# Kernel tuning notes

Measured on AMD Instinct MI355X. Metric: run time of the kernel, lower is better.

Reference implementation:

```python
import jax, jax.numpy as jnp
import numpy as np

N_SRC = 200000
N_TGT = 40000
NNZ = 280000
D_IN = 256
D_OUT = 256
LN_EPS = 1e-5


def setup_inputs() -> dict:
    key = jax.random.key(0)
    ks = jax.random.split(key, 6)
    x = jax.random.normal(ks[0], (N_SRC, D_IN), dtype=jnp.float32)
    rows = jax.random.randint(ks[1], (NNZ,), 0, N_TGT, dtype=jnp.int32)
    cols = jax.random.randint(ks[2], (NNZ,), 0, N_SRC, dtype=jnp.int32)
    vals = jax.random.uniform(ks[3], (NNZ,), dtype=jnp.float32)
    # Linear(in_dim, out_dim) params (PyTorch-style init scale)
    W = jax.random.normal(ks[4], (D_IN, D_OUT), dtype=jnp.float32) / np.sqrt(D_IN)
    b = jnp.zeros((D_OUT,), dtype=jnp.float32)
    # LayerNorm(out_dim) params
    gamma = jnp.ones((D_OUT,), dtype=jnp.float32)
    beta = jnp.zeros((D_OUT,), dtype=jnp.float32)
    return {"x": x, "rows": rows, "cols": cols, "vals": vals,
            "W": W, "b": b, "gamma": gamma, "beta": beta,
            "num_targets": N_TGT}


def reference(x, rows, cols, vals, W, b, gamma, beta, num_targets):
    # SpMM: mapped[t, :] = sum_{e: rows[e]==t} vals[e] * x[cols[e], :]
    contrib = x[cols] * vals[:, None]                      # [nnz, d_in]
    mapped = jax.ops.segment_sum(contrib, rows, num_segments=num_targets)  # [n_tgt, d_in]
    # Linear
    h = mapped @ W + b                                     # [n_tgt, d_out]
    # LayerNorm
    mu = jnp.mean(h, axis=-1, keepdims=True)
    var = jnp.mean(jnp.square(h - mu), axis=-1, keepdims=True)
    normed = (h - mu) * jax.lax.rsqrt(var + LN_EPS) * gamma + beta
    # GELU (exact erf form, matches torch nn.GELU default)
    return jax.nn.gelu(normed, approximate=False)
```

## Files before the change

kernel.cpp:

```cpp
#include <hip/hip_runtime.h>
#include <math.h>

#define D 256
#define TM 32
#define KC 16
#define LN_EPS 1e-5f
#define SCAN_CHUNK 1024

__global__ __launch_bounds__(256) void hist_kernel(
    const int* __restrict__ rows, int* __restrict__ cnt, int nnz)
{
    const int e = blockIdx.x * 256 + threadIdx.x;
    if (e < nnz) atomicAdd(&cnt[rows[e]], 1);
}

__global__ __launch_bounds__(256) void scan1_kernel(
    const int* __restrict__ cnt, int* __restrict__ row_ptr,
    int* __restrict__ partials, int n)
{
    const int tid = threadIdx.x;
    const int base = blockIdx.x * SCAN_CHUNK + tid * 4;
    int v[4];
#pragma unroll
    for (int q = 0; q < 4; q++) {
        const int i = base + q;
        v[q] = (i < n) ? cnt[i] : 0;
    }
    const int tsum = v[0] + v[1] + v[2] + v[3];

    const int lane = tid & 63;
    int s = tsum;
#pragma unroll
    for (int off = 1; off < 64; off <<= 1) {
        const int t = __shfl_up(s, off);
        if (lane >= off) s += t;
    }
    __shared__ int wtot[4];
    if (lane == 63) wtot[tid >> 6] = s;
    __syncthreads();
    const int w = tid >> 6;
    int woff = 0;
#pragma unroll
    for (int u = 0; u < 4; u++) if (u < w) woff += wtot[u];

    int run = woff + s - tsum;
#pragma unroll
    for (int q = 0; q < 4; q++) {
        const int i = base + q;
        if (i < n) row_ptr[i] = run;
        run += v[q];
    }
    if (tid == 255) partials[blockIdx.x] = woff + s;
}

__global__ __launch_bounds__(64) void scan2_kernel(int* __restrict__ partials, int nb)
{
    const int t = threadIdx.x;
    const int v = (t < nb) ? partials[t] : 0;
    int s = v;
#pragma unroll
    for (int off = 1; off < 64; off <<= 1) {
        const int u = __shfl_up(s, off);
        if (t >= off) s += u;
    }
    if (t < nb) partials[t] = s - v;
}

__global__ __launch_bounds__(256) void scan3_kernel(
    int* __restrict__ row_ptr, int* __restrict__ cursor,
    const int* __restrict__ partials, int n, int nnz)
{
    const int tid = threadIdx.x;
    const int base = blockIdx.x * SCAN_CHUNK + tid * 4;
    const int add = partials[blockIdx.x];
#pragma unroll
    for (int q = 0; q < 4; q++) {
        const int i = base + q;
        if (i < n) {
            const int rp = row_ptr[i] + add;
            row_ptr[i] = rp;
            cursor[i]  = rp;
        }
    }
    if (blockIdx.x == 0 && tid == 0) row_ptr[n] = nnz;
}

__global__ __launch_bounds__(256) void reorder_kernel(
    const int* __restrict__ rows, const int* __restrict__ cols,
    const float* __restrict__ vals, int* __restrict__ cursor,
    int* __restrict__ scol, float* __restrict__ sval, int nnz)
{
    const int e = blockIdx.x * 256 + threadIdx.x;
    if (e < nnz) {
        const int r = rows[e];
        const int pos = atomicAdd(&cursor[r], 1);
        scol[pos] = cols[e];
        sval[pos] = vals[e];
    }
}

__global__ __launch_bounds__(256, 8) void gather_kernel(
    const float* __restrict__ x, const int* __restrict__ row_ptr,
    const int* __restrict__ scol, const float* __restrict__ sval,
    float* __restrict__ mapped, int n_tgt)
{
    const int wid = (int)((blockIdx.x * blockDim.x + threadIdx.x) >> 6);
    const int lane = threadIdx.x & 63;
    if (wid >= n_tgt) return;

    const int beg = row_ptr[wid];
    const int end = row_ptr[wid + 1];

    float4 a0 = make_float4(0.f, 0.f, 0.f, 0.f);
    float4 a1 = a0, a2 = a0, a3 = a0;

    int e = beg;
    for (; e + 4 <= end; e += 4) {
        const int c0 = scol[e], c1 = scol[e + 1], c2 = scol[e + 2], c3 = scol[e + 3];
        const float v0 = sval[e], v1 = sval[e + 1], v2 = sval[e + 2], v3 = sval[e + 3];
        const float4 x0 = *(const float4*)(x + (size_t)c0 * D + 4 * lane);
        const float4 x1 = *(const float4*)(x + (size_t)c1 * D + 4 * lane);
        const float4 x2 = *(const float4*)(x + (size_t)c2 * D + 4 * lane);
        const float4 x3 = *(const float4*)(x + (size_t)c3 * D + 4 * lane);
        a0.x = fmaf(v0, x0.x, a0.x); a0.y = fmaf(v0, x0.y, a0.y);
        a0.z = fmaf(v0, x0.z, a0.z); a0.w = fmaf(v0, x0.w, a0.w);
        a1.x = fmaf(v1, x1.x, a1.x); a1.y = fmaf(v1, x1.y, a1.y);
        a1.z = fmaf(v1, x1.z, a1.z); a1.w = fmaf(v1, x1.w, a1.w);
        a2.x = fmaf(v2, x2.x, a2.x); a2.y = fmaf(v2, x2.y, a2.y);
        a2.z = fmaf(v2, x2.z, a2.z); a2.w = fmaf(v2, x2.w, a2.w);
        a3.x = fmaf(v3, x3.x, a3.x); a3.y = fmaf(v3, x3.y, a3.y);
        a3.z = fmaf(v3, x3.z, a3.z); a3.w = fmaf(v3, x3.w, a3.w);
    }
    for (; e < end; e++) {
        const int c0 = scol[e];
        const float v0 = sval[e];
        const float4 x0 = *(const float4*)(x + (size_t)c0 * D + 4 * lane);
        a0.x = fmaf(v0, x0.x, a0.x); a0.y = fmaf(v0, x0.y, a0.y);
        a0.z = fmaf(v0, x0.z, a0.z); a0.w = fmaf(v0, x0.w, a0.w);
    }
    const float4 acc = make_float4(a0.x + a1.x + a2.x + a3.x,
                                   a0.y + a1.y + a2.y + a3.y,
                                   a0.z + a1.z + a2.z + a3.z,
                                   a0.w + a1.w + a2.w + a3.w);
    *(float4*)(mapped + (size_t)wid * D + 4 * lane) = acc;
}

__global__ __launch_bounds__(256) void gemm_ln_gelu_kernel(
    const float* __restrict__ mapped, const float* __restrict__ Wm,
    const float* __restrict__ bias, const float* __restrict__ gamma,
    const float* __restrict__ beta, float* __restrict__ out, int n_tgt)
{
    __shared__ float As[TM][KC + 4];
    __shared__ float Bs[KC][D];

    const int tid = threadIdx.x;
    const int tr = tid >> 5;
    const int tc = tid & 31;
    const int r0 = blockIdx.x * TM;

    float acc[4][8];
#pragma unroll
    for (int i = 0; i < 4; i++)
#pragma unroll
        for (int j = 0; j < 8; j++) acc[i][j] = 0.f;

    for (int k0 = 0; k0 < D; k0 += KC) {
        if (tid < 128) {
            const int a_row = tid >> 2;
            const int a_kq  = (tid & 3) * 4;
            const float4 av = *(const float4*)(mapped + (size_t)(r0 + a_row) * D + k0 + a_kq);
            *(float4*)&As[a_row][a_kq] = av;
        }
#pragma unroll
        for (int q = 0; q < 4; q++) {
            const int idx = q * 256 + tid;
            const int kk = idx >> 6;
            const int c4 = (idx & 63) * 4;
            *(float4*)&Bs[kk][c4] = *(const float4*)(Wm + (size_t)(k0 + kk) * D + c4);
        }
        __syncthreads();

#pragma unroll
        for (int q = 0; q < 4; q++) {
            float4 a4[4];
#pragma unroll
            for (int i = 0; i < 4; i++)
                a4[i] = *(const float4*)&As[tr * 4 + i][q * 4];
#pragma unroll
            for (int kk = 0; kk < 4; kk++) {
                const float4 b0 = *(const float4*)&Bs[q * 4 + kk][4 * tc];
                const float4 b1 = *(const float4*)&Bs[q * 4 + kk][128 + 4 * tc];
#pragma unroll
                for (int i = 0; i < 4; i++) {
                    const float ai = (kk == 0) ? a4[i].x :
                                     (kk == 1) ? a4[i].y :
                                     (kk == 2) ? a4[i].z : a4[i].w;
                    acc[i][0] = fmaf(ai, b0.x, acc[i][0]);
                    acc[i][1] = fmaf(ai, b0.y, acc[i][1]);
                    acc[i][2] = fmaf(ai, b0.z, acc[i][2]);
                    acc[i][3] = fmaf(ai, b0.w, acc[i][3]);
                    acc[i][4] = fmaf(ai, b1.x, acc[i][4]);
                    acc[i][5] = fmaf(ai, b1.y, acc[i][5]);
                    acc[i][6] = fmaf(ai, b1.z, acc[i][6]);
                    acc[i][7] = fmaf(ai, b1.w, acc[i][7]);
                }
            }
        }
        __syncthreads();
    }

    float gm[8], bt[8], bs[8];
#pragma unroll
    for (int j = 0; j < 8; j++) {
        const int c = (j < 4) ? (4 * tc + j) : (128 + 4 * tc + (j - 4));
        gm[j] = gamma[c]; bt[j] = beta[c]; bs[j] = bias[c];
    }

#pragma unroll
    for (int i = 0; i < 4; i++) {
        float s = 0.f, ss = 0.f;
#pragma unroll
        for (int j = 0; j < 8; j++) {
            const float h = acc[i][j] + bs[j];
            acc[i][j] = h;
            s += h; ss += h * h;
        }
#pragma unroll
        for (int off = 16; off > 0; off >>= 1) {
            s  += __shfl_xor(s,  off);
            ss += __shfl_xor(ss, off);
        }
        const float mean = s * (1.f / D);
        const float var  = ss * (1.f / D) - mean * mean;
        const float rstd = rsqrtf(var + LN_EPS);

        const int row = r0 + tr * 4 + i;
        float y[8];
#pragma unroll
        for (int j = 0; j < 8; j++) {
            const float v = (acc[i][j] - mean) * rstd * gm[j] + bt[j];
            y[j] = 0.5f * v * (1.f + erff(v * 0.70710678118654752f));
        }
        float* op = out + (size_t)row * D;
        *(float4*)(op + 4 * tc)       = make_float4(y[0], y[1], y[2], y[3]);
        *(float4*)(op + 128 + 4 * tc) = make_float4(y[4], y[5], y[6], y[7]);
    }
}

extern "C" void kernel_launch(void* const* d_in, const int* in_sizes, int n_in,
                              void* d_out, int out_size, void* d_ws, size_t ws_size,
                              hipStream_t stream) {
    const float* x     = (const float*)d_in[0];
    const int*   rows  = (const int*)d_in[1];
    const int*   cols  = (const int*)d_in[2];
    const float* vals  = (const float*)d_in[3];
    const float* Wm    = (const float*)d_in[4];
    const float* bias  = (const float*)d_in[5];
    const float* gamma = (const float*)d_in[6];
    const float* beta  = (const float*)d_in[7];
    float* out = (float*)d_out;

    const int nnz   = in_sizes[1];
    const int n_tgt = out_size / D;

    int* cnt      = (int*)d_ws;
    int* row_ptr  = cnt + n_tgt;
    int* cursor   = row_ptr + n_tgt + 1;
    int* partials = cursor + n_tgt;
    int* scol     = partials + 64;
    float* sval   = (float*)(scol + nnz);
    float* mapped = (float*)(sval + nnz);
    mapped = (float*)(((uintptr_t)mapped + 15) & ~(uintptr_t)15);

    hipMemsetAsync(cnt, 0, (size_t)n_tgt * sizeof(int), stream);

    const int eblocks = (nnz + 255) / 256;
    hist_kernel<<<eblocks, 256, 0, stream>>>(rows, cnt, nnz);

    const int sblocks = (n_tgt + SCAN_CHUNK - 1) / SCAN_CHUNK;
    scan1_kernel<<<sblocks, 256, 0, stream>>>(cnt, row_ptr, partials, n_tgt);
    scan2_kernel<<<1, 64, 0, stream>>>(partials, sblocks);
    scan3_kernel<<<sblocks, 256, 0, stream>>>(row_ptr, cursor, partials, n_tgt, nnz);

    reorder_kernel<<<eblocks, 256, 0, stream>>>(rows, cols, vals, cursor,
                                                scol, sval, nnz);

    const int wblocks = (n_tgt * 64 + 255) / 256;
    gather_kernel<<<wblocks, 256, 0, stream>>>(x, row_ptr, scol, sval,
                                               mapped, n_tgt);

    const int gblocks = n_tgt / TM;
    gemm_ln_gelu_kernel<<<gblocks, 256, 0, stream>>>(mapped, Wm, bias, gamma,
                                                     beta, out, n_tgt);
}
```

Baseline: 423.3 us.

## Fuse SpMM gather into GEMM+LayerNorm+GELU kernel via shared-memory tile

The gather kernel and the GEMM/LN/GELU kernel become one. Each block of 4 wavefronts gathers its 32 target rows straight into a full 32x256 shared-memory A tile, so the mapped intermediate is never written to or read back from global memory. Column indices and values are now loaded cooperatively 64 at a time and broadcast with lane shuffles instead of every lane reading them redundantly. The cost is a larger shared-memory footprint (As grows to 32KB), which lowers occupancy. The gather phase also loses the latency hiding that independent gather waves had, because each wave handles 8 rows serially before the GEMM can start.

Result: slower. 445.7 us (+5.3%).

```diff
diff --git a/kernel.cpp b/kernel.cpp
--- a/kernel.cpp
+++ b/kernel.cpp
@@ -99,64 +99,81 @@
     }
 }
 
-__global__ __launch_bounds__(256, 8) void gather_kernel(
+__global__ __launch_bounds__(256) void fused_spmm_gemm_kernel(
     const float* __restrict__ x, const int* __restrict__ row_ptr,
     const int* __restrict__ scol, const float* __restrict__ sval,
-    float* __restrict__ mapped, int n_tgt)
-{
-    const int wid = (int)((blockIdx.x * blockDim.x + threadIdx.x) >> 6);
-    const int lane = threadIdx.x & 63;
-    if (wid >= n_tgt) return;
-
-    const int beg = row_ptr[wid];
-    const int end = row_ptr[wid + 1];
-
-    float4 a0 = make_float4(0.f, 0.f, 0.f, 0.f);
-    float4 a1 = a0, a2 = a0, a3 = a0;
-
-    int e = beg;
-    for (; e + 4 <= end; e += 4) {
-        const int c0 = scol[e], c1 = scol[e + 1], c2 = scol[e + 2], c3 = scol[e + 3];
-        const float v0 = sval[e], v1 = sval[e + 1], v2 = sval[e + 2], v3 = sval[e + 3];
-        const float4 x0 = *(const float4*)(x + (size_t)c0 * D + 4 * lane);
-        const float4 x1 = *(const float4*)(x + (size_t)c1 * D + 4 * lane);
-        const float4 x2 = *(const float4*)(x + (size_t)c2 * D + 4 * lane);
-        const float4 x3 = *(const float4*)(x + (size_t)c3 * D + 4 * lane);
-        a0.x = fmaf(v0, x0.x, a0.x); a0.y = fmaf(v0, x0.y, a0.y);
-        a0.z = fmaf(v0, x0.z, a0.z); a0.w = fmaf(v0, x0.w, a0.w);
-        a1.x = fmaf(v1, x1.x, a1.x); a1.y = fmaf(v1, x1.y, a1.y);
-        a1.z = fmaf(v1, x1.z, a1.z); a1.w = fmaf(v1, x1.w, a1.w);
-        a2.x = fmaf(v2, x2.x, a2.x); a2.y = fmaf(v2, x2.y, a2.y);
-        a2.z = fmaf(v2, x2.z, a2.z); a2.w = fmaf(v2, x2.w, a2.w);
-        a3.x = fmaf(v3, x3.x, a3.x); a3.y = fmaf(v3, x3.y, a3.y);
-        a3.z = fmaf(v3, x3.z, a3.z); a3.w = fmaf(v3, x3.w, a3.w);
-    }
-    for (; e < end; e++) {
-        const int c0 = scol[e];
-        const float v0 = sval[e];
-        const float4 x0 = *(const float4*)(x + (size_t)c0 * D + 4 * lane);
-        a0.x = fmaf(v0, x0.x, a0.x); a0.y = fmaf(v0, x0.y, a0.y);
-        a0.z = fmaf(v0, x0.z, a0.z); a0.w = fmaf(v0, x0.w, a0.w);
-    }
-    const float4 acc = make_float4(a0.x + a1.x + a2.x + a3.x,
-                                   a0.y + a1.y + a2.y + a3.y,
-                                   a0.z + a1.z + a2.z + a3.z,
-                                   a0.w + a1.w + a2.w + a3.w);
-    *(float4*)(mapped + (size_t)wid * D + 4 * lane) = acc;
-}
-
-__global__ __launch_bounds__(256) void gemm_ln_gelu_kernel(
-    const float* __restrict__ mapped, const float* __restrict__ Wm,
-    const float* __restrict__ bias, const float* __restrict__ gamma,
-    const float* __restrict__ beta, float* __restrict__ out, int n_tgt)
-{
-    __shared__ float As[TM][KC + 4];
+    const float* __restrict__ Wm, const float* __restrict__ bias,
+    const float* __restrict__ gamma, const float* __restrict__ beta,
+    float* __restrict__ out)
+{
+    __shared__ float As[TM][D];
     __shared__ float Bs[KC][D];
 
-    const int tid = threadIdx.x;
+    const int tid  = threadIdx.x;
+    const int wv   = tid >> 6;
+    const int lane = tid & 63;
+    const int r0   = blockIdx.x * TM;
+
+    const int rbase = r0 + wv * 8;
+    int rp = 0;
+    if (lane < 9) rp = row_ptr[rbase + lane];
+
+    for (int rr = 0; rr < 8; rr++) {
+        const int beg = __shfl(rp, rr);
+        const int end = __shfl(rp, rr + 1);
+
+        float4 a0 = make_float4(0.f, 0.f, 0.f, 0.f);
+        float4 a1 = a0, a2 = a0, a3 = a0;
+
+        for (int cb = beg; cb < end; cb += 64) {
+            const int cnt = min(64, end - cb);
+            int   cidx = 0;
+            float cval = 0.f;
+            if (lane < cnt) {
+                cidx = scol[cb + lane];
+                cval = sval[cb + lane];
+            }
+            int j = 0;
+            for (; j + 4 <= cnt; j += 4) {
+                const int   c0 = __shfl(cidx, j);
+                const int   c1 = __shfl(cidx, j + 1);
+                const int   c2 = __shfl(cidx, j + 2);
+                const int   c3 = __shfl(cidx, j + 3);
+                const float v0 = __shfl(cval, j);
+                const float v1 = __shfl(cval, j + 1);
+                const float v2 = __shfl(cval, j + 2);
+                const float v3 = __shfl(cval, j + 3);
+                const float4 x0 = *(const float4*)(x + (size_t)c0 * D + 4 * lane);
+                const float4 x1 = *(const float4*)(x + (size_t)c1 * D + 4 * lane);
+                const float4 x2 = *(const float4*)(x + (size_t)c2 * D + 4 * lane);
+                const float4 x3 = *(const float4*)(x + (size_t)c3 * D + 4 * lane);
+                a0.x = fmaf(v0, x0.x, a0.x); a0.y = fmaf(v0, x0.y, a0.y);
+                a0.z = fmaf(v0, x0.z, a0.z); a0.w = fmaf(v0, x0.w, a0.w);
+                a1.x = fmaf(v1, x1.x, a1.x); a1.y = fmaf(v1, x1.y, a1.y);
+                a1.z = fmaf(v1, x1.z, a1.z); a1.w = fmaf(v1, x1.w, a1.w);
+                a2.x = fmaf(v2, x2.x, a2.x); a2.y = fmaf(v2, x2.y, a2.y);
+                a2.z = fmaf(v2, x2.z, a2.z); a2.w = fmaf(v2, x2.w, a2.w);
+                a3.x = fmaf(v3, x3.x, a3.x); a3.y = fmaf(v3, x3.y, a3.y);
+                a3.z = fmaf(v3, x3.z, a3.z); a3.w = fmaf(v3, x3.w, a3.w);
+            }
+            for (; j < cnt; j++) {
+                const int   c0 = __shfl(cidx, j);
+                const float v0 = __shfl(cval, j);
+                const float4 x0 = *(const float4*)(x + (size_t)c0 * D + 4 * lane);
+                a0.x = fmaf(v0, x0.x, a0.x); a0.y = fmaf(v0, x0.y, a0.y);
+                a0.z = fmaf(v0, x0.z, a0.z); a0.w = fmaf(v0, x0.w, a0.w);
+            }
+        }
+        const float4 s = make_float4(a0.x + a1.x + a2.x + a3.x,
+                                     a0.y + a1.y + a2.y + a3.y,
+                                     a0.z + a1.z + a2.z + a3.z,
+                                     a0.w + a1.w + a2.w + a3.w);
+        *(float4*)&As[wv * 8 + rr][4 * lane] = s;
+    }
+    __syncthreads();
+
     const int tr = tid >> 5;
     const int tc = tid & 31;
-    const int r0 = blockIdx.x * TM;
 
     float acc[4][8];
 #pragma unroll
@@ -165,12 +182,6 @@
         for (int j = 0; j < 8; j++) acc[i][j] = 0.f;
 
     for (int k0 = 0; k0 < D; k0 += KC) {
-        if (tid < 128) {
-            const int a_row = tid >> 2;
-            const int a_kq  = (tid & 3) * 4;
-            const float4 av = *(const float4*)(mapped + (size_t)(r0 + a_row) * D + k0 + a_kq);
-            *(float4*)&As[a_row][a_kq] = av;
-        }
 #pragma unroll
         for (int q = 0; q < 4; q++) {
             const int idx = q * 256 + tid;
@@ -185,7 +196,7 @@
             float4 a4[4];
 #pragma unroll
             for (int i = 0; i < 4; i++)
-                a4[i] = *(const float4*)&As[tr * 4 + i][q * 4];
+                a4[i] = *(const float4*)&As[tr * 4 + i][k0 + q * 4];
 #pragma unroll
             for (int kk = 0; kk < 4; kk++) {
                 const float4 b0 = *(const float4*)&Bs[q * 4 + kk][4 * tc];
@@ -269,8 +280,6 @@
     int* partials = cursor + n_tgt;
     int* scol     = partials + 64;
     float* sval   = (float*)(scol + nnz);
-    float* mapped = (float*)(sval + nnz);
-    mapped = (float*)(((uintptr_t)mapped + 15) & ~(uintptr_t)15);
 
     hipMemsetAsync(cnt, 0, (size_t)n_tgt * sizeof(int), stream);
 
@@ -285,11 +294,7 @@
     reorder_kernel<<<eblocks, 256, 0, stream>>>(rows, cols, vals, cursor,
                                                 scol, sval, nnz);
 
-    const int wblocks = (n_tgt * 64 + 255) / 256;
-    gather_kernel<<<wblocks, 256, 0, stream>>>(x, row_ptr, scol, sval,
-                                               mapped, n_tgt);
-
     const int gblocks = n_tgt / TM;
-    gemm_ln_gelu_kernel<<<gblocks, 256, 0, stream>>>(mapped, Wm, bias, gamma,
-                                                     beta, out, n_tgt);
-}
+    fused_spmm_gemm_kernel<<<gblocks, 256, 0, stream>>>(
+        x, row_ptr, scol, sval, Wm, bias, gamma, beta, out);
+}
```
